# Optimization experiments

Hardware: AMD Instinct MI355X
Metric: run time of the kernel (lower is better)

The kernel has to match this reference:

```python
import jax, jax.numpy as jnp
import numpy as np

NUM_EXPERTS = 8
TOP_K = 2


def setup_inputs() -> dict:
    key = jax.random.key(0)
    k1, k2, k3, k4, k5 = jax.random.split(key, 5)
    H, F, E = 1024, 4096, NUM_EXPERTS
    s = 0.02
    return {
        "hidden_states": jax.random.normal(k1, (2, 2048, H), jnp.float32),
        "w_router": jax.random.normal(k2, (E, H), jnp.float32) * s,
        "w1": jax.random.normal(k3, (E, F, H), jnp.float32) * s,
        "w2": jax.random.normal(k4, (E, H, F), jnp.float32) * s,
        "w3": jax.random.normal(k5, (E, F, H), jnp.float32) * s,
    }


def reference(hidden_states, w_router, w1, w2, w3):
    B, S, H = hidden_states.shape
    x = hidden_states.reshape(-1, H)  # [T, H]
    T = x.shape[0]
    # router (nn.Linear, no bias): logits = x @ W^T
    router_logits = x @ w_router.T  # [T, E]
    probs = jax.nn.softmax(router_logits.astype(jnp.float32), axis=-1)
    top_w, top_e = jax.lax.top_k(probs, TOP_K)  # [T, K]
    top_w = top_w / jnp.sum(top_w, axis=-1, keepdims=True)
    top_w = top_w.astype(x.dtype)
    # dense per-token gate matrix [T, E]; zero where expert not selected
    gates = jnp.zeros((T, NUM_EXPERTS), x.dtype).at[
        jnp.arange(T)[:, None], top_e
    ].add(top_w)
    out = jnp.zeros_like(x)
    for e in range(NUM_EXPERTS):  # fixed small expert loop
        h = jax.nn.silu(x @ w1[e].T) * (x @ w3[e].T)  # [T, F]
        out = out + gates[:, e:e + 1] * (h @ w2[e].T)
    return out.reshape(B, S, H), router_logits
```

## Files before the change

kernel.cpp:

```cpp
#include <hip/hip_runtime.h>
#include <hip/hip_bf16.h>
#include <stdint.h>

#define T_TOK 4096
#define H_DIM 1024
#define F_DIM 4096
#define NE 8
#define MG_BLKS 40

typedef float    f32x4  __attribute__((ext_vector_type(4)));
typedef __bf16   bf16x8 __attribute__((ext_vector_type(8)));
typedef uint16_t u16x8  __attribute__((ext_vector_type(8)));

#define AS1 __attribute__((address_space(1)))
#define AS3 __attribute__((address_space(3)))

__device__ __forceinline__ uint16_t f2bf(float f) {
  return __builtin_bit_cast(uint16_t, __float2bfloat16(f));
}

__device__ __forceinline__ void gld16(const void* g, void* l) {
  __builtin_amdgcn_global_load_lds((const AS1 void*)g, (AS3 void*)l, 16, 0, 0);
}

__global__ __launch_bounds__(256) void cvt_k(const float* __restrict__ src,
                                             uint16_t* __restrict__ dst, int n8) {
  const int stride = gridDim.x * blockDim.x;
  for (int i = blockIdx.x * blockDim.x + threadIdx.x; i < n8; i += stride) {
    const float* s = src + (size_t)i * 8;
    f32x4 a = *(const f32x4*)s;
    f32x4 b = *(const f32x4*)(s + 4);
    u16x8 o;
#pragma unroll
    for (int j = 0; j < 4; ++j) { o[j] = f2bf(a[j]); o[j + 4] = f2bf(b[j]); }
    *(u16x8*)(dst + (size_t)i * 8) = o;
  }
}

__global__ __launch_bounds__(256) void router_k(
    const float* __restrict__ x, const float* __restrict__ wr,
    float* __restrict__ logits, uint16_t* __restrict__ xb,
    int* __restrict__ pairTok, float* __restrict__ pairGate,
    int* __restrict__ tokSlot, int* __restrict__ cnt)
{
  const int lane = threadIdx.x & 63;
  const int wid  = threadIdx.x >> 6;
  const int t    = blockIdx.x * 4 + wid;

  const float* xp = x + (size_t)t * H_DIM + lane * 16;
  f32x4 xv[4];
#pragma unroll
  for (int i = 0; i < 4; ++i) xv[i] = *(const f32x4*)(xp + 4 * i);

  u16x8 o0, o1;
#pragma unroll
  for (int j = 0; j < 4; ++j) {
    o0[j] = f2bf(xv[0][j]); o0[j + 4] = f2bf(xv[1][j]);
    o1[j] = f2bf(xv[2][j]); o1[j + 4] = f2bf(xv[3][j]);
  }
  uint16_t* xbp = xb + (size_t)t * H_DIM + lane * 16;
  *(u16x8*)xbp       = o0;
  *(u16x8*)(xbp + 8) = o1;

  float s[NE];
#pragma unroll
  for (int e = 0; e < NE; ++e) {
    const float* wp = wr + e * H_DIM + lane * 16;
    float acc = 0.f;
#pragma unroll
    for (int i = 0; i < 4; ++i) {
      f32x4 wv = *(const f32x4*)(wp + 4 * i);
#pragma unroll
      for (int j = 0; j < 4; ++j) acc += xv[i][j] * wv[j];
    }
#pragma unroll
    for (int off = 32; off > 0; off >>= 1) acc += __shfl_xor(acc, off, 64);
    s[e] = acc;
  }

  if (lane == 0) {
#pragma unroll
    for (int e = 0; e < NE; ++e) logits[t * NE + e] = s[e];
    int e1 = 0;
#pragma unroll
    for (int e = 1; e < NE; ++e) if (s[e] > s[e1]) e1 = e;
    int e2 = (e1 == 0) ? 1 : 0;
#pragma unroll
    for (int e = 0; e < NE; ++e)
      if (e != e1 && e != e2 && s[e] > s[e2]) e2 = e;
    const float d  = s[e2] - s[e1];
    const float g1 = 1.f / (1.f + __expf(d));
    const float g2 = 1.f - g1;
    int i1 = atomicAdd(cnt + e1, 1);
    pairTok[e1 * T_TOK + i1] = t;  pairGate[e1 * T_TOK + i1] = g1;
    int i2 = atomicAdd(cnt + e2, 1);
    pairTok[e2 * T_TOK + i2] = t;  pairGate[e2 * T_TOK + i2] = g2;
    int4 sl; sl.x = e1; sl.y = i1; sl.z = e2; sl.w = i2;
    ((int4*)tokSlot)[t] = sl;
  }
}

__global__ void prefix_k(const int* __restrict__ cnt, int* __restrict__ base) {
  if (threadIdx.x == 0) {
    int b = 0;
#pragma unroll
    for (int e = 0; e < NE; ++e) { base[e] = b; b += (cnt[e] + 255) & ~255; }
    base[NE] = b;
  }
}


__global__ __launch_bounds__(256, 2) void ffn1b_k(
    const uint16_t* __restrict__ xb, const uint16_t* __restrict__ w1b,
    const uint16_t* __restrict__ w3b, uint16_t* __restrict__ hbuf,
    const int* __restrict__ pairTok, const float* __restrict__ pairGate,
    const int* __restrict__ cnt, const int* __restrict__ base)
{
  const int mg0 = blockIdx.y * 256;
  if (mg0 >= base[NE]) return;
  int e = 0;
#pragma unroll
  for (int k = 1; k < NE; ++k) if (mg0 >= base[k]) e = k;
  const int m0   = mg0 - base[e];
  const int cnte = cnt[e];
  const int n0   = blockIdx.x * 64;
  const int tid  = threadIdx.x;
  const int lane = tid & 63;
  const int wid  = tid >> 6;
  const int wm   = (wid >> 1) * 128;
  const int wn   = (wid & 1) * 32;

  __shared__ __align__(16) uint16_t lsA [256 * 64];
  __shared__ __align__(16) uint16_t lsB1[ 64 * 64];
  __shared__ __align__(16) uint16_t lsB3[ 64 * 64];
  __shared__ float lsG[256];

  {
    const int rr = m0 + tid;
    lsG[tid] = (rr < cnte) ? pairGate[e * T_TOK + rr] : 0.f;
  }

  const uint16_t* w1e = w1b + (size_t)e * F_DIM * H_DIM;
  const uint16_t* w3e = w3b + (size_t)e * F_DIM * H_DIM;

  const uint16_t* asrc[8];
#pragma unroll
  for (int q = 0; q < 8; ++q) {
    const int c = q * 256 + tid;
    const int row = c >> 3, pos = c & 7;
    const int kc  = pos ^ (row & 7);
    int ar = m0 + row; if (ar >= cnte) ar = cnte - 1;
    const int tok = pairTok[e * T_TOK + ar];
    asrc[q] = xb + (size_t)tok * H_DIM + kc * 8;
  }
  const uint16_t* b1src[2];
  const uint16_t* b3src[2];
#pragma unroll
  for (int q = 0; q < 2; ++q) {
    const int c = q * 256 + tid;
    const int row = c >> 3, pos = c & 7;
    const int kc  = pos ^ (row & 7);
    b1src[q] = w1e + (size_t)(n0 + row) * H_DIM + kc * 8;
    b3src[q] = w3e + (size_t)(n0 + row) * H_DIM + kc * 8;
  }

  const f32x4 fz = {0.f, 0.f, 0.f, 0.f};
  f32x4 acc1[8][2], acc3[8][2];
#pragma unroll
  for (int i = 0; i < 8; ++i)
#pragma unroll
    for (int j = 0; j < 2; ++j) { acc1[i][j] = fz; acc3[i][j] = fz; }

  for (int kt = 0; kt < H_DIM; kt += 64) {
    __syncthreads();
#pragma unroll
    for (int q = 0; q < 8; ++q)
      gld16(asrc[q] + kt, &lsA[(q * 256 + tid) * 8]);
#pragma unroll
    for (int q = 0; q < 2; ++q) {
      gld16(b1src[q] + kt, &lsB1[(q * 256 + tid) * 8]);
      gld16(b3src[q] + kt, &lsB3[(q * 256 + tid) * 8]);
    }
    __syncthreads();
#pragma unroll
    for (int ks = 0; ks < 2; ++ks) {
      const int kg = ks * 4 + (lane >> 4);
      bf16x8 af[8], b1f[2], b3f[2];
#pragma unroll
      for (int i = 0; i < 8; ++i) {
        const int ar = wm + i * 16 + (lane & 15);
        af[i] = *(const bf16x8*)&lsA[ar * 64 + ((kg ^ (ar & 7)) * 8)];
      }
#pragma unroll
      for (int j = 0; j < 2; ++j) {
        const int br = wn + j * 16 + (lane & 15);
        b1f[j] = *(const bf16x8*)&lsB1[br * 64 + ((kg ^ (br & 7)) * 8)];
        b3f[j] = *(const bf16x8*)&lsB3[br * 64 + ((kg ^ (br & 7)) * 8)];
      }
#pragma unroll
      for (int i = 0; i < 8; ++i)
#pragma unroll
        for (int j = 0; j < 2; ++j) {
          acc1[i][j] = __builtin_amdgcn_mfma_f32_16x16x32_bf16(af[i], b1f[j], acc1[i][j], 0, 0, 0);
          acc3[i][j] = __builtin_amdgcn_mfma_f32_16x16x32_bf16(af[i], b3f[j], acc3[i][j], 0, 0, 0);
        }
    }
  }

  const int be = base[e];
#pragma unroll
  for (int i = 0; i < 8; ++i) {
#pragma unroll
    for (int r = 0; r < 4; ++r) {
      const int lrow = m0 + wm + i * 16 + (lane >> 4) * 4 + r;
      if (lrow < cnte) {
        const float g = lsG[lrow - m0];
        uint16_t* hp = hbuf + (size_t)(be + lrow) * F_DIM + n0 + wn + (lane & 15);
#pragma unroll
        for (int j = 0; j < 2; ++j) {
          const float a  = acc1[i][j][r];
          const float hv = g * (a / (1.f + __expf(-a))) * acc3[i][j][r];
          hp[j * 16] = f2bf(hv);
        }
      }
    }
  }
}

__global__ __launch_bounds__(256, 2) void ffn2b_k(
    const uint16_t* __restrict__ hbuf, const uint16_t* __restrict__ w2b,
    uint16_t* __restrict__ y, const int* __restrict__ cnt,
    const int* __restrict__ base)
{
  const int mg0 = blockIdx.y * 256;
  if (mg0 >= base[NE]) return;
  int e = 0;
#pragma unroll
  for (int k = 1; k < NE; ++k) if (mg0 >= base[k]) e = k;
  const int m0   = mg0 - base[e];
  const int cnte = cnt[e];
  const int n0   = blockIdx.x * 128;
  const int tid  = threadIdx.x;
  const int lane = tid & 63;
  const int wid  = tid >> 6;
  const int wm   = (wid >> 1) * 128;
  const int wn   = (wid & 1) * 64;

  __shared__ __align__(16) uint16_t lsA[256 * 64];
  __shared__ __align__(16) uint16_t lsB[128 * 64];

  const int be = base[e];
  const uint16_t* w2e = w2b + (size_t)e * H_DIM * F_DIM;

  const uint16_t* asrc[8];
#pragma unroll
  for (int q = 0; q < 8; ++q) {
    const int c = q * 256 + tid;
    const int row = c >> 3, pos = c & 7;
    const int kc  = pos ^ (row & 7);
    int rr = m0 + row; if (rr >= cnte) rr = cnte - 1;
    asrc[q] = hbuf + (size_t)(be + rr) * F_DIM + kc * 8;
  }
  const uint16_t* bsrc[4];
#pragma unroll
  for (int q = 0; q < 4; ++q) {
    const int c = q * 256 + tid;
    const int row = c >> 3, pos = c & 7;
    const int kc  = pos ^ (row & 7);
    bsrc[q] = w2e + (size_t)(n0 + row) * F_DIM + kc * 8;
  }

  const f32x4 fz = {0.f, 0.f, 0.f, 0.f};
  f32x4 acc[8][4];
#pragma unroll
  for (int i = 0; i < 8; ++i)
#pragma unroll
    for (int j = 0; j < 4; ++j) acc[i][j] = fz;

  for (int kt = 0; kt < F_DIM; kt += 64) {
    __syncthreads();
#pragma unroll
    for (int q = 0; q < 8; ++q)
      gld16(asrc[q] + kt, &lsA[(q * 256 + tid) * 8]);
#pragma unroll
    for (int q = 0; q < 4; ++q)
      gld16(bsrc[q] + kt, &lsB[(q * 256 + tid) * 8]);
    __syncthreads();
#pragma unroll
    for (int ks = 0; ks < 2; ++ks) {
      const int kg = ks * 4 + (lane >> 4);
      bf16x8 af[8], bf[4];
#pragma unroll
      for (int i = 0; i < 8; ++i) {
        const int ar = wm + i * 16 + (lane & 15);
        af[i] = *(const bf16x8*)&lsA[ar * 64 + ((kg ^ (ar & 7)) * 8)];
      }
#pragma unroll
      for (int j = 0; j < 4; ++j) {
        const int br = wn + j * 16 + (lane & 15);
        bf[j] = *(const bf16x8*)&lsB[br * 64 + ((kg ^ (br & 7)) * 8)];
      }
#pragma unroll
      for (int i = 0; i < 8; ++i)
#pragma unroll
        for (int j = 0; j < 4; ++j)
          acc[i][j] = __builtin_amdgcn_mfma_f32_16x16x32_bf16(af[i], bf[j], acc[i][j], 0, 0, 0);
    }
  }

#pragma unroll
  for (int i = 0; i < 8; ++i) {
#pragma unroll
    for (int r = 0; r < 4; ++r) {
      const int lrow = m0 + wm + i * 16 + (lane >> 4) * 4 + r;
      if (lrow < cnte) {
        uint16_t* yp = y + (size_t)(be + lrow) * H_DIM + n0 + wn + (lane & 15);
#pragma unroll
        for (int j = 0; j < 4; ++j)
          yp[j * 16] = f2bf(acc[i][j][r]);
      }
    }
  }
}


__global__ __launch_bounds__(256, 2) void ffn1_k(
    const uint16_t* __restrict__ xb, const float* __restrict__ w1,
    const float* __restrict__ w3, uint16_t* __restrict__ hbuf,
    const int* __restrict__ pairTok, const float* __restrict__ pairGate,
    const int* __restrict__ cnt, const int* __restrict__ base)
{
  const int mg0 = blockIdx.y * 256;
  if (mg0 >= base[NE]) return;
  int e = 0;
#pragma unroll
  for (int k = 1; k < NE; ++k) if (mg0 >= base[k]) e = k;
  const int m0   = mg0 - base[e];
  const int cnte = cnt[e];
  const int n0   = blockIdx.x * 64;
  const int tid  = threadIdx.x;
  const int lane = tid & 63;
  const int wid  = tid >> 6;
  const int wm   = (wid >> 1) * 128;
  const int wn   = (wid & 1) * 32;

  __shared__ __align__(16) uint16_t lsA [256 * 64];
  __shared__ __align__(16) uint16_t lsB1[ 64 * 64];
  __shared__ __align__(16) uint16_t lsB3[ 64 * 64];
  __shared__ float lsG[256];

  {
    const int rr = m0 + tid;
    lsG[tid] = (rr < cnte) ? pairGate[e * T_TOK + rr] : 0.f;
  }

  const float* w1e = w1 + (size_t)e * F_DIM * H_DIM;
  const float* w3e = w3 + (size_t)e * F_DIM * H_DIM;

  const uint16_t* asrc[8];
#pragma unroll
  for (int q = 0; q < 8; ++q) {
    const int c = q * 256 + tid;
    const int row = c >> 3, pos = c & 7;
    const int kc  = pos ^ (row & 7);
    int ar = m0 + row; if (ar >= cnte) ar = cnte - 1;
    const int tok = pairTok[e * T_TOK + ar];
    asrc[q] = xb + (size_t)tok * H_DIM + kc * 8;
  }
  const float* b1src[2];
  const float* b3src[2];
  int bdst[2];
#pragma unroll
  for (int q = 0; q < 2; ++q) {
    const int c = q * 256 + tid;
    const int row = c >> 3, pos = c & 7;
    const int kc  = pos ^ (row & 7);
    bdst[q] = c * 8;
    b1src[q] = w1e + (size_t)(n0 + row) * H_DIM + kc * 8;
    b3src[q] = w3e + (size_t)(n0 + row) * H_DIM + kc * 8;
  }

  const f32x4 fz = {0.f, 0.f, 0.f, 0.f};
  f32x4 acc1[8][2], acc3[8][2];
#pragma unroll
  for (int i = 0; i < 8; ++i)
#pragma unroll
    for (int j = 0; j < 2; ++j) { acc1[i][j] = fz; acc3[i][j] = fz; }

  for (int kt = 0; kt < H_DIM; kt += 64) {
    __syncthreads();
#pragma unroll
    for (int q = 0; q < 8; ++q)
      gld16(asrc[q] + kt, &lsA[(q * 256 + tid) * 8]);
#pragma unroll
    for (int q = 0; q < 2; ++q) {
      const float* s1 = b1src[q] + kt;
      const float* s3 = b3src[q] + kt;
      f32x4 a0 = *(const f32x4*)s1;
      f32x4 a1 = *(const f32x4*)(s1 + 4);
      f32x4 c0 = *(const f32x4*)s3;
      f32x4 c1 = *(const f32x4*)(s3 + 4);
      u16x8 ob1, ob3;
#pragma unroll
      for (int j = 0; j < 4; ++j) {
        ob1[j] = f2bf(a0[j]); ob1[j + 4] = f2bf(a1[j]);
        ob3[j] = f2bf(c0[j]); ob3[j + 4] = f2bf(c1[j]);
      }
      *(u16x8*)&lsB1[bdst[q]] = ob1;
      *(u16x8*)&lsB3[bdst[q]] = ob3;
    }
    __syncthreads();
#pragma unroll
    for (int ks = 0; ks < 2; ++ks) {
      const int kg = ks * 4 + (lane >> 4);
      bf16x8 af[8], b1f[2], b3f[2];
#pragma unroll
      for (int i = 0; i < 8; ++i) {
        const int ar = wm + i * 16 + (lane & 15);
        af[i] = *(const bf16x8*)&lsA[ar * 64 + ((kg ^ (ar & 7)) * 8)];
      }
#pragma unroll
      for (int j = 0; j < 2; ++j) {
        const int br = wn + j * 16 + (lane & 15);
        b1f[j] = *(const bf16x8*)&lsB1[br * 64 + ((kg ^ (br & 7)) * 8)];
        b3f[j] = *(const bf16x8*)&lsB3[br * 64 + ((kg ^ (br & 7)) * 8)];
      }
#pragma unroll
      for (int i = 0; i < 8; ++i)
#pragma unroll
        for (int j = 0; j < 2; ++j) {
          acc1[i][j] = __builtin_amdgcn_mfma_f32_16x16x32_bf16(af[i], b1f[j], acc1[i][j], 0, 0, 0);
          acc3[i][j] = __builtin_amdgcn_mfma_f32_16x16x32_bf16(af[i], b3f[j], acc3[i][j], 0, 0, 0);
        }
    }
  }

  const int be = base[e];
#pragma unroll
  for (int i = 0; i < 8; ++i) {
#pragma unroll
    for (int r = 0; r < 4; ++r) {
      const int lrow = m0 + wm + i * 16 + (lane >> 4) * 4 + r;
      if (lrow < cnte) {
        const float g = lsG[lrow - m0];
        uint16_t* hp = hbuf + (size_t)(be + lrow) * F_DIM + n0 + wn + (lane & 15);
#pragma unroll
        for (int j = 0; j < 2; ++j) {
          const float a  = acc1[i][j][r];
          const float hv = g * (a / (1.f + __expf(-a))) * acc3[i][j][r];
          hp[j * 16] = f2bf(hv);
        }
      }
    }
  }
}

__global__ __launch_bounds__(256, 2) void ffn2_k(
    const uint16_t* __restrict__ hbuf, const float* __restrict__ w2,
    uint16_t* __restrict__ y, const int* __restrict__ cnt,
    const int* __restrict__ base)
{
  const int mg0 = blockIdx.y * 256;
  if (mg0 >= base[NE]) return;
  int e = 0;
#pragma unroll
  for (int k = 1; k < NE; ++k) if (mg0 >= base[k]) e = k;
  const int m0   = mg0 - base[e];
  const int cnte = cnt[e];
  const int n0   = blockIdx.x * 128;
  const int tid  = threadIdx.x;
  const int lane = tid & 63;
  const int wid  = tid >> 6;
  const int wm   = (wid >> 1) * 128;
  const int wn   = (wid & 1) * 64;

  __shared__ __align__(16) uint16_t lsA[256 * 64];
  __shared__ __align__(16) uint16_t lsB[128 * 64];

  const int be = base[e];
  const float* w2e = w2 + (size_t)e * H_DIM * F_DIM;

  const uint16_t* asrc[8];
#pragma unroll
  for (int q = 0; q < 8; ++q) {
    const int c = q * 256 + tid;
    const int row = c >> 3, pos = c & 7;
    const int kc  = pos ^ (row & 7);
    int rr = m0 + row; if (rr >= cnte) rr = cnte - 1;
    asrc[q] = hbuf + (size_t)(be + rr) * F_DIM + kc * 8;
  }
  const float* bsrc[4];
  int bdst[4];
#pragma unroll
  for (int q = 0; q < 4; ++q) {
    const int c = q * 256 + tid;
    const int row = c >> 3, pos = c & 7;
    const int kc  = pos ^ (row & 7);
    bdst[q] = c * 8;
    bsrc[q] = w2e + (size_t)(n0 + row) * F_DIM + kc * 8;
  }

  const f32x4 fz = {0.f, 0.f, 0.f, 0.f};
  f32x4 acc[8][4];
#pragma unroll
  for (int i = 0; i < 8; ++i)
#pragma unroll
    for (int j = 0; j < 4; ++j) acc[i][j] = fz;

  for (int kt = 0; kt < F_DIM; kt += 64) {
    __syncthreads();
#pragma unroll
    for (int q = 0; q < 8; ++q)
      gld16(asrc[q] + kt, &lsA[(q * 256 + tid) * 8]);
#pragma unroll
    for (int q = 0; q < 4; ++q) {
      const float* sb = bsrc[q] + kt;
      f32x4 b0 = *(const f32x4*)sb;
      f32x4 b1 = *(const f32x4*)(sb + 4);
      u16x8 ob;
#pragma unroll
      for (int j = 0; j < 4; ++j) { ob[j] = f2bf(b0[j]); ob[j + 4] = f2bf(b1[j]); }
      *(u16x8*)&lsB[bdst[q]] = ob;
    }
    __syncthreads();
#pragma unroll
    for (int ks = 0; ks < 2; ++ks) {
      const int kg = ks * 4 + (lane >> 4);
      bf16x8 af[8], bf[4];
#pragma unroll
      for (int i = 0; i < 8; ++i) {
        const int ar = wm + i * 16 + (lane & 15);
        af[i] = *(const bf16x8*)&lsA[ar * 64 + ((kg ^ (ar & 7)) * 8)];
      }
#pragma unroll
      for (int j = 0; j < 4; ++j) {
        const int br = wn + j * 16 + (lane & 15);
        bf[j] = *(const bf16x8*)&lsB[br * 64 + ((kg ^ (br & 7)) * 8)];
      }
#pragma unroll
      for (int i = 0; i < 8; ++i)
#pragma unroll
        for (int j = 0; j < 4; ++j)
          acc[i][j] = __builtin_amdgcn_mfma_f32_16x16x32_bf16(af[i], bf[j], acc[i][j], 0, 0, 0);
    }
  }

#pragma unroll
  for (int i = 0; i < 8; ++i) {
#pragma unroll
    for (int r = 0; r < 4; ++r) {
      const int lrow = m0 + wm + i * 16 + (lane >> 4) * 4 + r;
      if (lrow < cnte) {
        uint16_t* yp = y + (size_t)(be + lrow) * H_DIM + n0 + wn + (lane & 15);
#pragma unroll
        for (int j = 0; j < 4; ++j)
          yp[j * 16] = f2bf(acc[i][j][r]);
      }
    }
  }
}

__global__ __launch_bounds__(256) void combine_k(
    const uint16_t* __restrict__ y, const int* __restrict__ tokSlot,
    const int* __restrict__ base, float* __restrict__ out)
{
  const int t = blockIdx.x * 2 + (threadIdx.x >> 7);
  const int c = (threadIdx.x & 127) * 8;
  const int4 s = ((const int4*)tokSlot)[t];
  const uint16_t* y1 = y + (size_t)(base[s.x] + s.y) * H_DIM + c;
  const uint16_t* y2 = y + (size_t)(base[s.z] + s.w) * H_DIM + c;
  const u16x8 a = *(const u16x8*)y1;
  const u16x8 b = *(const u16x8*)y2;
  float* op = out + (size_t)t * H_DIM + c;
  f32x4 o0, o1;
#pragma unroll
  for (int j = 0; j < 4; ++j) {
    o0[j] = __bfloat162float(__hip_bfloat16_raw{a[j]}) +
            __bfloat162float(__hip_bfloat16_raw{b[j]});
    o1[j] = __bfloat162float(__hip_bfloat16_raw{a[j + 4]}) +
            __bfloat162float(__hip_bfloat16_raw{b[j + 4]});
  }
  *(f32x4*)op       = o0;
  *(f32x4*)(op + 4) = o1;
}

extern "C" void kernel_launch(void* const* d_in, const int* in_sizes, int n_in,
                              void* d_out, int out_size, void* d_ws, size_t ws_size,
                              hipStream_t stream)
{
  const float* x  = (const float*)d_in[0];
  const float* wr = (const float*)d_in[1];
  const float* w1 = (const float*)d_in[2];
  const float* w2 = (const float*)d_in[3];
  const float* w3 = (const float*)d_in[4];
  float* out    = (float*)d_out;
  float* logits = out + (size_t)T_TOK * H_DIM;

  uint8_t* ws = (uint8_t*)d_ws;
  const size_t PADROWS  = (size_t)MG_BLKS * 256;
  const size_t WELEMS   = (size_t)NE * F_DIM * H_DIM;
  const size_t XB_OFF   = 0;
  const size_t HB_OFF   = XB_OFF + (size_t)T_TOK * H_DIM * 2;
  const size_t Y_OFF    = HB_OFF + PADROWS * F_DIM * 2;
  const size_t PT_OFF   = Y_OFF + PADROWS * H_DIM * 2;
  const size_t PG_OFF   = PT_OFF + (size_t)NE * T_TOK * 4;
  const size_t TS_OFF   = PG_OFF + (size_t)NE * T_TOK * 4;
  const size_t CNT_OFF  = TS_OFF + (size_t)T_TOK * 16;
  const size_t BASE_OFF = CNT_OFF + 64;
  const size_t W1B_OFF  = (BASE_OFF + 64 + 255) & ~(size_t)255;
  const size_t W3B_OFF  = W1B_OFF + WELEMS * 2;
  const size_t W2B_OFF  = W3B_OFF + WELEMS * 2;
  const size_t NEED_BIG = W2B_OFF + WELEMS * 2;
  const size_t NEED_SM  = W1B_OFF;
  if (ws_size < NEED_SM) return;

  uint16_t* xb      = (uint16_t*)(ws + XB_OFF);
  uint16_t* hb      = (uint16_t*)(ws + HB_OFF);
  uint16_t* yb      = (uint16_t*)(ws + Y_OFF);
  int*      pairTok = (int*)(ws + PT_OFF);
  float*    pairGate= (float*)(ws + PG_OFF);
  int*      tokSlot = (int*)(ws + TS_OFF);
  int*      cnt     = (int*)(ws + CNT_OFF);
  int*      basep   = (int*)(ws + BASE_OFF);

  hipMemsetAsync(cnt, 0, 64, stream);
  router_k<<<T_TOK / 4, 256, 0, stream>>>(x, wr, logits, xb, pairTok, pairGate, tokSlot, cnt);
  prefix_k<<<1, 64, 0, stream>>>(cnt, basep);

  if (ws_size >= NEED_BIG) {
    uint16_t* w1b = (uint16_t*)(ws + W1B_OFF);
    uint16_t* w3b = (uint16_t*)(ws + W3B_OFF);
    uint16_t* w2b = (uint16_t*)(ws + W2B_OFF);
    const int n8 = (int)(WELEMS / 8);
    cvt_k<<<2048, 256, 0, stream>>>(w1, w1b, n8);
    cvt_k<<<2048, 256, 0, stream>>>(w3, w3b, n8);
    cvt_k<<<2048, 256, 0, stream>>>(w2, w2b, n8);
    ffn1b_k<<<dim3(F_DIM / 64, MG_BLKS, 1), 256, 0, stream>>>(xb, w1b, w3b, hb, pairTok, pairGate, cnt, basep);
    ffn2b_k<<<dim3(H_DIM / 128, MG_BLKS, 1), 256, 0, stream>>>(hb, w2b, yb, cnt, basep);
  } else {
    ffn1_k<<<dim3(F_DIM / 64, MG_BLKS, 1), 256, 0, stream>>>(xb, w1, w3, hb, pairTok, pairGate, cnt, basep);
    ffn2_k<<<dim3(H_DIM / 128, MG_BLKS, 1), 256, 0, stream>>>(hb, w2, yb, cnt, basep);
  }
  combine_k<<<T_TOK / 2, 256, 0, stream>>>(yb, tokSlot, basep, out);
}
```

Baseline: 525.2 us.

## Double-buffer ffn1b LDS tiles and widen block to 512 threads, 128 cols

The gate/up GEMM kernel now uses 512-thread blocks covering 128 output columns (8 waves), so each A tile loaded from gathered tokens is reused across twice as many columns. It also double-buffers the LDS tiles, prefetching two k-steps ahead with vmcnt waits and raw barriers so global loads overlap the MFMA work. The gate values are read straight from global memory in the epilogue instead of being staged in LDS. LDS use roughly doubles to about 128KB per block, which forces one block per CU and lowers occupancy. The hand-set vmcnt counts must match the number of loads issued per stage.

After: 542.5 us. +3.3%, slower.

```diff
diff --git a/kernel.cpp b/kernel.cpp
--- a/kernel.cpp
+++ b/kernel.cpp
@@ -110,7 +110,7 @@
 }
 
 
-__global__ __launch_bounds__(256, 2) void ffn1b_k(
+__global__ __launch_bounds__(512, 1) void ffn1b_k(
     const uint16_t* __restrict__ xb, const uint16_t* __restrict__ w1b,
     const uint16_t* __restrict__ w3b, uint16_t* __restrict__ hbuf,
     const int* __restrict__ pairTok, const float* __restrict__ pairGate,
@@ -123,30 +123,24 @@
   for (int k = 1; k < NE; ++k) if (mg0 >= base[k]) e = k;
   const int m0   = mg0 - base[e];
   const int cnte = cnt[e];
-  const int n0   = blockIdx.x * 64;
+  const int n0   = blockIdx.x * 128;
   const int tid  = threadIdx.x;
   const int lane = tid & 63;
   const int wid  = tid >> 6;
-  const int wm   = (wid >> 1) * 128;
-  const int wn   = (wid & 1) * 32;
-
-  __shared__ __align__(16) uint16_t lsA [256 * 64];
-  __shared__ __align__(16) uint16_t lsB1[ 64 * 64];
-  __shared__ __align__(16) uint16_t lsB3[ 64 * 64];
-  __shared__ float lsG[256];
-
-  {
-    const int rr = m0 + tid;
-    lsG[tid] = (rr < cnte) ? pairGate[e * T_TOK + rr] : 0.f;
-  }
+  const int wm   = (wid >> 2) * 128;
+  const int wn   = (wid & 3) * 32;
+
+  __shared__ __align__(16) uint16_t lsA [2][256 * 64];
+  __shared__ __align__(16) uint16_t lsB1[2][128 * 64];
+  __shared__ __align__(16) uint16_t lsB3[2][128 * 64];
 
   const uint16_t* w1e = w1b + (size_t)e * F_DIM * H_DIM;
   const uint16_t* w3e = w3b + (size_t)e * F_DIM * H_DIM;
 
-  const uint16_t* asrc[8];
-#pragma unroll
-  for (int q = 0; q < 8; ++q) {
-    const int c = q * 256 + tid;
+  const uint16_t* asrc[4];
+#pragma unroll
+  for (int q = 0; q < 4; ++q) {
+    const int c = q * 512 + tid;
     const int row = c >> 3, pos = c & 7;
     const int kc  = pos ^ (row & 7);
     int ar = m0 + row; if (ar >= cnte) ar = cnte - 1;
@@ -157,13 +151,45 @@
   const uint16_t* b3src[2];
 #pragma unroll
   for (int q = 0; q < 2; ++q) {
-    const int c = q * 256 + tid;
+    const int c = q * 512 + tid;
     const int row = c >> 3, pos = c & 7;
     const int kc  = pos ^ (row & 7);
     b1src[q] = w1e + (size_t)(n0 + row) * H_DIM + kc * 8;
     b3src[q] = w3e + (size_t)(n0 + row) * H_DIM + kc * 8;
   }
 
+#define STAGE1(buf, koff)                                                 \
+  {                                                                       \
+    _Pragma("unroll") for (int q = 0; q < 4; ++q)                         \
+      gld16(asrc[q] + (koff), &lsA[buf][(q * 512 + tid) * 8]);            \
+    _Pragma("unroll") for (int q = 0; q < 2; ++q) {                       \
+      gld16(b1src[q] + (koff), &lsB1[buf][(q * 512 + tid) * 8]);          \
+      gld16(b3src[q] + (koff), &lsB3[buf][(q * 512 + tid) * 8]);          \
+    }                                                                     \
+  }
+
+#define COMPUTE1(cur)                                                     \
+  {                                                                       \
+    _Pragma("unroll") for (int ks = 0; ks < 2; ++ks) {                    \
+      const int kg = ks * 4 + (lane >> 4);                                \
+      bf16x8 af[8], b1f[2], b3f[2];                                       \
+      _Pragma("unroll") for (int i = 0; i < 8; ++i) {                     \
+        const int ar = wm + i * 16 + (lane & 15);                         \
+        af[i] = *(const bf16x8*)&lsA[cur][ar * 64 + ((kg ^ (ar & 7)) * 8)]; \
+      }                                                                   \
+      _Pragma("unroll") for (int j = 0; j < 2; ++j) {                     \
+        const int br = wn + j * 16 + (lane & 15);                         \
+        b1f[j] = *(const bf16x8*)&lsB1[cur][br * 64 + ((kg ^ (br & 7)) * 8)]; \
+        b3f[j] = *(const bf16x8*)&lsB3[cur][br * 64 + ((kg ^ (br & 7)) * 8)]; \
+      }                                                                   \
+      _Pragma("unroll") for (int i = 0; i < 8; ++i)                       \
+        _Pragma("unroll") for (int j = 0; j < 2; ++j) {                   \
+          acc1[i][j] = __builtin_amdgcn_mfma_f32_16x16x32_bf16(af[i], b1f[j], acc1[i][j], 0, 0, 0); \
+          acc3[i][j] = __builtin_amdgcn_mfma_f32_16x16x32_bf16(af[i], b3f[j], acc3[i][j], 0, 0, 0); \
+        }                                                                 \
+    }                                                                     \
+  }
+
   const f32x4 fz = {0.f, 0.f, 0.f, 0.f};
   f32x4 acc1[8][2], acc3[8][2];
 #pragma unroll
@@ -171,41 +197,25 @@
 #pragma unroll
     for (int j = 0; j < 2; ++j) { acc1[i][j] = fz; acc3[i][j] = fz; }
 
-  for (int kt = 0; kt < H_DIM; kt += 64) {
-    __syncthreads();
-#pragma unroll
-    for (int q = 0; q < 8; ++q)
-      gld16(asrc[q] + kt, &lsA[(q * 256 + tid) * 8]);
-#pragma unroll
-    for (int q = 0; q < 2; ++q) {
-      gld16(b1src[q] + kt, &lsB1[(q * 256 + tid) * 8]);
-      gld16(b3src[q] + kt, &lsB3[(q * 256 + tid) * 8]);
-    }
-    __syncthreads();
-#pragma unroll
-    for (int ks = 0; ks < 2; ++ks) {
-      const int kg = ks * 4 + (lane >> 4);
-      bf16x8 af[8], b1f[2], b3f[2];
-#pragma unroll
-      for (int i = 0; i < 8; ++i) {
-        const int ar = wm + i * 16 + (lane & 15);
-        af[i] = *(const bf16x8*)&lsA[ar * 64 + ((kg ^ (ar & 7)) * 8)];
-      }
-#pragma unroll
-      for (int j = 0; j < 2; ++j) {
-        const int br = wn + j * 16 + (lane & 15);
-        b1f[j] = *(const bf16x8*)&lsB1[br * 64 + ((kg ^ (br & 7)) * 8)];
-        b3f[j] = *(const bf16x8*)&lsB3[br * 64 + ((kg ^ (br & 7)) * 8)];
-      }
-#pragma unroll
-      for (int i = 0; i < 8; ++i)
-#pragma unroll
-        for (int j = 0; j < 2; ++j) {
-          acc1[i][j] = __builtin_amdgcn_mfma_f32_16x16x32_bf16(af[i], b1f[j], acc1[i][j], 0, 0, 0);
-          acc3[i][j] = __builtin_amdgcn_mfma_f32_16x16x32_bf16(af[i], b3f[j], acc3[i][j], 0, 0, 0);
-        }
-    }
-  }
+  const int NT = H_DIM / 64;
+  STAGE1(0, 0)
+  STAGE1(1, 64)
+
+  for (int t = 0; t < NT - 1; ++t) {
+    const int cur = t & 1;
+    asm volatile("s_waitcnt vmcnt(8)" ::: "memory");
+    __builtin_amdgcn_s_barrier();
+    COMPUTE1(cur)
+    __builtin_amdgcn_s_barrier();
+    if (t + 2 < NT) STAGE1(cur, (t + 2) * 64)
+  }
+  {
+    asm volatile("s_waitcnt vmcnt(0)" ::: "memory");
+    __builtin_amdgcn_s_barrier();
+    COMPUTE1((NT - 1) & 1)
+  }
+#undef STAGE1
+#undef COMPUTE1
 
   const int be = base[e];
 #pragma unroll
@@ -214,7 +224,7 @@
     for (int r = 0; r < 4; ++r) {
       const int lrow = m0 + wm + i * 16 + (lane >> 4) * 4 + r;
       if (lrow < cnte) {
-        const float g = lsG[lrow - m0];
+        const float g = pairGate[e * T_TOK + lrow];
         uint16_t* hp = hbuf + (size_t)(be + lrow) * F_DIM + n0 + wn + (lane & 15);
 #pragma unroll
         for (int j = 0; j < 2; ++j) {
@@ -635,7 +645,7 @@
     cvt_k<<<2048, 256, 0, stream>>>(w1, w1b, n8);
     cvt_k<<<2048, 256, 0, stream>>>(w3, w3b, n8);
     cvt_k<<<2048, 256, 0, stream>>>(w2, w2b, n8);
-    ffn1b_k<<<dim3(F_DIM / 64, MG_BLKS, 1), 256, 0, stream>>>(xb, w1b, w3b, hb, pairTok, pairGate, cnt, basep);
+    ffn1b_k<<<dim3(F_DIM / 128, MG_BLKS, 1), 512, 0, stream>>>(xb, w1b, w3b, hb, pairTok, pairGate, cnt, basep);
     ffn2b_k<<<dim3(H_DIM / 128, MG_BLKS, 1), 256, 0, stream>>>(hb, w2b, yb, cnt, basep);
   } else {
     ffn1_k<<<dim3(F_DIM / 64, MG_BLKS, 1), 256, 0, stream>>>(xb, w1, w3, hb, pairTok, pairGate, cnt, basep);
```
